# Kernel tuning notes

Measured on AMD Instinct MI355X. Metric: run time of the kernel, lower is better.

Reference implementation:

```python
import jax, jax.numpy as jnp
import numpy as np

B, D_IN, D_OUT, E, K, H = 8192, 1024, 1024, 8, 2, 2048


def setup_inputs() -> dict:
    key = jax.random.key(0)
    ks = jax.random.split(key, 7)
    s_in = 1.0 / np.sqrt(D_IN)
    s_h = 1.0 / np.sqrt(H)
    return {
        "x": jax.random.normal(ks[0], (B, D_IN), dtype=jnp.float32),
        "Wg": jax.random.uniform(ks[1], (D_IN, E), minval=-s_in, maxval=s_in, dtype=jnp.float32),
        "bg": jax.random.uniform(ks[2], (E,), minval=-s_in, maxval=s_in, dtype=jnp.float32),
        "W1": jax.random.uniform(ks[3], (E, D_IN, H), minval=-s_in, maxval=s_in, dtype=jnp.float32),
        "b1": jax.random.uniform(ks[4], (E, H), minval=-s_in, maxval=s_in, dtype=jnp.float32),
        "W2": jax.random.uniform(ks[5], (E, H, D_OUT), minval=-s_h, maxval=s_h, dtype=jnp.float32),
        "b2": jax.random.uniform(ks[6], (E, D_OUT), minval=-s_h, maxval=s_h, dtype=jnp.float32),
    }


def reference(x, Wg, bg, W1, b1, W2, b2):
    # gating: linear then top-k -> binary mask (scores are NOT used as weights)
    gate_scores = x @ Wg + bg                      # [B, E]
    _, topk_idx = jax.lax.top_k(gate_scores, K)    # [B, K]
    mask = jax.nn.one_hot(topk_idx, E, dtype=x.dtype).sum(axis=-2)  # [B, E]

    # dense compute of ALL experts (faithful to original module)
    h = jax.nn.relu(jnp.einsum('bi,eih->beh', x, W1) + b1[None])    # [B, E, H]
    expert_out = jnp.einsum('beh,eho->beo', h, W2) + b2[None]       # [B, E, D_OUT]

    # mask to top-k experts and sum over experts
    return jnp.einsum('beo,be->bo', expert_out, mask)               # [B, D_OUT]
```

## Files before the change

### kernel.cpp

```cpp
#include <hip/hip_runtime.h>


#define NTOK 8192
#define DIN  1024
#define DOUT 1024
#define NEXP 8
#define NHID 2048
#define NENT (NTOK * 2)
#define ABLK 64
#define MCHMAX 72

typedef __bf16 bf16_t;
typedef __bf16 bf16x8 __attribute__((ext_vector_type(8)));
typedef __bf16 bf16x4 __attribute__((ext_vector_type(4)));
typedef float  f32x4  __attribute__((ext_vector_type(4)));

#define AS3(p) ((__attribute__((address_space(3))) void*)(unsigned)(unsigned long long)(p))
#define AS1(p) ((__attribute__((address_space(1))) void*)(unsigned long long)(p))

static __device__ __forceinline__ int imin_(int a, int b) { return a < b ? a : b; }

static __device__ __forceinline__ int xcd_swizzle() {
    int cpx = gridDim.x >> 3;
    return (blockIdx.x & 7) * cpx + (blockIdx.x >> 3);
}

__global__ __launch_bounds__(256) void k_transpose_cvt(
    const float* __restrict__ W, bf16_t* __restrict__ WT, int K_, int N_)
{
    __shared__ float tile[64][65];
    const int tilesK = K_ >> 6, tilesN = N_ >> 6;
    int bid = blockIdx.x;
    int e = bid / (tilesK * tilesN);
    int r = bid % (tilesK * tilesN);
    int tk = (r / tilesN) << 6;
    int tn = (r % tilesN) << 6;
    const float* Wb  = W  + (size_t)e * K_ * N_;
    bf16_t*      WTb = WT + (size_t)e * K_ * N_;
    int lr = threadIdx.x >> 6;
    int lc = threadIdx.x & 63;
#pragma unroll
    for (int i = 0; i < 16; ++i) {
        int row = i * 4 + lr;
        tile[row][lc] = Wb[(size_t)(tk + row) * N_ + tn + lc];
    }
    __syncthreads();
#pragma unroll
    for (int i = 0; i < 16; ++i) {
        int row = i * 4 + lr;
        WTb[(size_t)(tn + row) * K_ + tk + lc] = (bf16_t)tile[lc][row];
    }
}

__global__ __launch_bounds__(256) void k_wgT(
    const float* __restrict__ Wg, float* __restrict__ WgT)
{
    int i = blockIdx.x * 256 + threadIdx.x;
    int d = i >> 3, e = i & 7;
    WgT[e * DIN + d] = Wg[i];
}

__global__ __launch_bounds__(256) void k_gating(
    const float* __restrict__ x, const float* __restrict__ WgT,
    const float* __restrict__ bg, bf16_t* __restrict__ xb,
    int* __restrict__ topk)
{
    int lane = threadIdx.x & 63;
    int tok  = blockIdx.x * 4 + (threadIdx.x >> 6);
    const float* xr  = x  + (size_t)tok * DIN;
    bf16_t*      xbr = xb + (size_t)tok * DIN;

    float4 xv[4];
#pragma unroll
    for (int i = 0; i < 4; ++i) {
        int idx = i * 256 + lane * 4;
        xv[i] = *reinterpret_cast<const float4*>(xr + idx);
        bf16x4 o;
        o[0] = (bf16_t)xv[i].x; o[1] = (bf16_t)xv[i].y;
        o[2] = (bf16_t)xv[i].z; o[3] = (bf16_t)xv[i].w;
        *reinterpret_cast<bf16x4*>(xbr + idx) = o;
    }

    float acc[NEXP];
#pragma unroll
    for (int e = 0; e < NEXP; ++e) {
        const float* we = WgT + (size_t)e * DIN;
        float a = 0.f;
#pragma unroll
        for (int i = 0; i < 4; ++i) {
            int idx = i * 256 + lane * 4;
            float4 w = *reinterpret_cast<const float4*>(we + idx);
            a += xv[i].x * w.x + xv[i].y * w.y + xv[i].z * w.z + xv[i].w * w.w;
        }
        acc[e] = a;
    }

#pragma unroll
    for (int e = 0; e < NEXP; ++e) {
#pragma unroll
        for (int off = 32; off >= 1; off >>= 1) acc[e] += __shfl_xor(acc[e], off);
    }
    if (lane == 0) {
        float s[NEXP];
#pragma unroll
        for (int e = 0; e < NEXP; ++e) s[e] = acc[e] + bg[e];
        int e0 = 0;
        for (int e = 1; e < NEXP; ++e) if (s[e] > s[e0]) e0 = e;
        int e1 = (e0 == 0) ? 1 : 0;
        for (int e = 0; e < NEXP; ++e) if (e != e0 && s[e] > s[e1]) e1 = e;
        topk[2 * tok]     = e0;
        topk[2 * tok + 1] = e1;
    }
}

__global__ __launch_bounds__(256) void k_hist(
    const int* __restrict__ topk, int* __restrict__ bh)
{
    __shared__ int h[NEXP];
    if (threadIdx.x < NEXP) h[threadIdx.x] = 0;
    __syncthreads();
    int i = blockIdx.x * 256 + threadIdx.x;
    atomicAdd(&h[topk[i]], 1);
    __syncthreads();
    if (threadIdx.x < NEXP) bh[blockIdx.x * NEXP + threadIdx.x] = h[threadIdx.x];
}

__global__ void k_scan2(const int* __restrict__ bh, int* __restrict__ counts,
                        int* __restrict__ offsets, int* __restrict__ blockbase,
                        int* __restrict__ chtab, int* __restrict__ nch)
{
    __shared__ int sc[NEXP], so_[NEXP + 1];
    int t = threadIdx.x;
    if (t < NEXP) {
        int s = 0;
        for (int b = 0; b < ABLK; ++b) s += bh[b * NEXP + t];
        sc[t] = s;
    }
    __syncthreads();
    if (t == 0) {
        int s = 0;
        for (int e = 0; e < NEXP; ++e) { so_[e] = s; s += sc[e]; }
        so_[NEXP] = s;
        for (int e = 0; e <= NEXP; ++e) offsets[e] = so_[e];
        for (int e = 0; e < NEXP; ++e) counts[e] = sc[e];
    }
    __syncthreads();
    if (t < NEXP) {
        int run = so_[t];
        for (int b = 0; b < ABLK; ++b) {
            blockbase[b * NEXP + t] = run;
            run += bh[b * NEXP + t];
        }
    }
    __syncthreads();
    if (t == 0) {
        int n = 0;
        for (int e = 0; e < NEXP; ++e) {
            int mch = (sc[e] + 255) >> 8;
            for (int m = 0; m < mch; ++m) chtab[n++] = (e << 16) | m;
        }
        nch[0] = n;
    }
}

__global__ __launch_bounds__(256) void k_assign(
    const int* __restrict__ topk, const int* __restrict__ blockbase,
    int* __restrict__ token_ids, int* __restrict__ slot_of)
{
    __shared__ int wcnt[4][NEXP];
    int tid = threadIdx.x, blk = blockIdx.x;
    int i = blk * 256 + tid;
    int e = topk[i];
    int lane = tid & 63, w = tid >> 6;
    unsigned long long ltmask = (1ull << lane) - 1ull;
    int rank_w = 0;
#pragma unroll
    for (int ee = 0; ee < NEXP; ++ee) {
        unsigned long long m = __ballot(e == ee);
        if (ee == e) rank_w = (int)__popcll(m & ltmask);
        if (lane == 0) wcnt[w][ee] = (int)__popcll(m);
    }
    __syncthreads();
    int pre = 0;
    for (int wv = 0; wv < w; ++wv) pre += wcnt[wv][e];
    int s = blockbase[blk * NEXP + e] + pre + rank_w;
    token_ids[s] = i >> 1;
    slot_of[i] = s;
}


#define GEMM_PHASES(NKV)                                                           \
    for (int kt = 0; kt < NKV; ++kt) {                                             \
        const short* Ac = &As[kt & 1][0][0];                                       \
        const short* Bc = &Bs[kt & 1][0][0];                                       \
        unsigned dstb = (unsigned)(((kt & 1) ^ 1) * 32768) + wb;                   \
        bf16x8 b_[4][2];                                                           \
        _Pragma("unroll")                                                          \
        for (int ph = 0; ph < 4; ++ph) {                                           \
            if (ph == 0) {                                                         \
                if (kt + 1 < NKV) {                                                \
                    int ko = (kt + 1) * 64;                                        \
                    __builtin_amdgcn_global_load_lds(AS1(aP0 + ko), AS3(AB + dstb),         16, 0, 0); \
                    __builtin_amdgcn_global_load_lds(AS1(aP1 + ko), AS3(AB + dstb + 8192),  16, 0, 0); \
                    __builtin_amdgcn_global_load_lds(AS1(aP2 + ko), AS3(AB + dstb + 16384), 16, 0, 0); \
                    __builtin_amdgcn_global_load_lds(AS1(aP3 + ko), AS3(AB + dstb + 24576), 16, 0, 0); \
                    __builtin_amdgcn_global_load_lds(AS1(bP0 + ko), AS3(BB + dstb),         16, 0, 0); \
                    __builtin_amdgcn_global_load_lds(AS1(bP1 + ko), AS3(BB + dstb + 8192),  16, 0, 0); \
                    __builtin_amdgcn_global_load_lds(AS1(bP2 + ko), AS3(BB + dstb + 16384), 16, 0, 0); \
                    __builtin_amdgcn_global_load_lds(AS1(bP3 + ko), AS3(BB + dstb + 24576), 16, 0, 0); \
                }                                                                  \
                _Pragma("unroll")                                                  \
                for (int nf = 0; nf < 4; ++nf) {                                   \
                    b_[nf][0] = *reinterpret_cast<const bf16x8*>(Bc + nf * 1024 + boff0);        \
                    b_[nf][1] = *reinterpret_cast<const bf16x8*>(Bc + nf * 1024 + (boff0 ^ 32)); \
                }                                                                  \
            }                                                                      \
            bf16x8 a_[2][2];                                                       \
            _Pragma("unroll")                                                      \
            for (int j = 0; j < 2; ++j) {                                          \
                const short* ar = Ac + (ph * 2 + j) * 1024;                        \
                a_[j][0] = *reinterpret_cast<const bf16x8*>(ar + aoff0);           \
                a_[j][1] = *reinterpret_cast<const bf16x8*>(ar + (aoff0 ^ 32));    \
            }                                                                      \
            __builtin_amdgcn_s_barrier();                                          \
            __builtin_amdgcn_s_setprio(1);                                         \
            _Pragma("unroll")                                                      \
            for (int j = 0; j < 2; ++j) {                                          \
                _Pragma("unroll")                                                  \
                for (int nf = 0; nf < 4; ++nf) {                                   \
                    acc[ph * 2 + j][nf] = __builtin_amdgcn_mfma_f32_16x16x32_bf16( \
                        a_[j][0], b_[nf][0], acc[ph * 2 + j][nf], 0, 0, 0);        \
                    acc[ph * 2 + j][nf] = __builtin_amdgcn_mfma_f32_16x16x32_bf16( \
                        a_[j][1], b_[nf][1], acc[ph * 2 + j][nf], 0, 0, 0);        \
                }                                                                  \
            }                                                                      \
            __builtin_amdgcn_s_setprio(0);                                         \
            if (ph == 3) asm volatile("s_waitcnt vmcnt(0)" ::: "memory");          \
            __builtin_amdgcn_s_barrier();                                          \
        }                                                                          \
    }

__global__ __launch_bounds__(512) void k_gemm1(
    const bf16_t* __restrict__ xb, const bf16_t* __restrict__ w1t,
    const float* __restrict__ b1, bf16_t* __restrict__ hb,
    const int* __restrict__ token_ids, const int* __restrict__ counts,
    const int* __restrict__ offsets, const int* __restrict__ chtab,
    const int* __restrict__ nch)
{
    int bid   = xcd_swizzle();
    int chunk = bid >> 3;
    int nc    = bid & 7;
    if (chunk >= nch[0]) return;
    int em = chtab[chunk];
    int e  = em >> 16;
    int mc = em & 0xffff;
    int count = counts[e];
    int base  = offsets[e];

    __shared__ short As[2][256][64];
    __shared__ short Bs[2][256][64];

    int t    = threadIdx.x;
    int w    = t >> 6;
    int lane = t & 63;
    int wrM  = (w >> 2) * 128;
    int wcN  = (w & 3) * 64;
    int lm   = lane & 15;
    int kq   = lane >> 4;
    int ru   = lane & 7;

    int aoff0 = (wrM + lm) * 64 + ((kq ^ ru) * 8);
    int boff0 = (wcN + lm) * 64 + ((kq ^ ru) * 8);

    int rbase = t >> 3;
    int c0s   = ((t & 7) ^ ((t >> 3) & 7)) * 8;
    unsigned wb = (unsigned)(w * 1024);

    const bf16_t* wgt = w1t + (size_t)e * NHID * DIN;
    int r0 = imin_(mc * 256 +   0 + rbase, count - 1);
    int r1 = imin_(mc * 256 +  64 + rbase, count - 1);
    int r2 = imin_(mc * 256 + 128 + rbase, count - 1);
    int r3 = imin_(mc * 256 + 192 + rbase, count - 1);
    const bf16_t* aP0 = xb + (size_t)token_ids[base + r0] * DIN + c0s;
    const bf16_t* aP1 = xb + (size_t)token_ids[base + r1] * DIN + c0s;
    const bf16_t* aP2 = xb + (size_t)token_ids[base + r2] * DIN + c0s;
    const bf16_t* aP3 = xb + (size_t)token_ids[base + r3] * DIN + c0s;
    const bf16_t* bP0 = wgt + (size_t)(nc * 256 +   0 + rbase) * DIN + c0s;
    const bf16_t* bP1 = wgt + (size_t)(nc * 256 +  64 + rbase) * DIN + c0s;
    const bf16_t* bP2 = wgt + (size_t)(nc * 256 + 128 + rbase) * DIN + c0s;
    const bf16_t* bP3 = wgt + (size_t)(nc * 256 + 192 + rbase) * DIN + c0s;

    char* AB = (char*)&As[0][0][0];
    char* BB = (char*)&Bs[0][0][0];

    f32x4 acc[8][4];
#pragma unroll
    for (int m = 0; m < 8; ++m)
#pragma unroll
        for (int n = 0; n < 4; ++n) acc[m][n] = (f32x4){0.f, 0.f, 0.f, 0.f};

    __builtin_amdgcn_global_load_lds(AS1(aP0), AS3(AB + wb),         16, 0, 0);
    __builtin_amdgcn_global_load_lds(AS1(aP1), AS3(AB + wb + 8192),  16, 0, 0);
    __builtin_amdgcn_global_load_lds(AS1(aP2), AS3(AB + wb + 16384), 16, 0, 0);
    __builtin_amdgcn_global_load_lds(AS1(aP3), AS3(AB + wb + 24576), 16, 0, 0);
    __builtin_amdgcn_global_load_lds(AS1(bP0), AS3(BB + wb),         16, 0, 0);
    __builtin_amdgcn_global_load_lds(AS1(bP1), AS3(BB + wb + 8192),  16, 0, 0);
    __builtin_amdgcn_global_load_lds(AS1(bP2), AS3(BB + wb + 16384), 16, 0, 0);
    __builtin_amdgcn_global_load_lds(AS1(bP3), AS3(BB + wb + 24576), 16, 0, 0);
    asm volatile("s_waitcnt vmcnt(0)" ::: "memory");
    __builtin_amdgcn_s_barrier();

    constexpr int NK = DIN / 64;
    GEMM_PHASES(NK)

    int rq = kq * 4;
#pragma unroll
    for (int nf = 0; nf < 4; ++nf) {
        int col  = nc * 256 + wcN + nf * 16 + lm;
        float bias = b1[e * NHID + col];
#pragma unroll
        for (int mf = 0; mf < 8; ++mf) {
            int gr0 = mc * 256 + wrM + mf * 16 + rq;
#pragma unroll
            for (int q = 0; q < 4; ++q) {
                int gr = gr0 + q;
                if (gr < count) {
                    float v = acc[mf][nf][q] + bias;
                    v = v > 0.f ? v : 0.f;
                    hb[(size_t)(base + gr) * NHID + col] = (bf16_t)v;
                }
            }
        }
    }
}

__global__ __launch_bounds__(512) void k_gemm2(
    const bf16_t* __restrict__ hb, const bf16_t* __restrict__ w2t,
    bf16_t* __restrict__ so,
    const int* __restrict__ counts, const int* __restrict__ offsets,
    const int* __restrict__ chtab, const int* __restrict__ nch)
{
    int bid   = xcd_swizzle();
    int chunk = bid >> 2;
    int nc    = bid & 3;
    if (chunk >= nch[0]) return;
    int em = chtab[chunk];
    int e  = em >> 16;
    int mc = em & 0xffff;
    int count = counts[e];
    int base  = offsets[e];

    __shared__ short As[2][256][64];
    __shared__ short Bs[2][256][64];

    int t    = threadIdx.x;
    int w    = t >> 6;
    int lane = t & 63;
    int wrM  = (w >> 2) * 128;
    int wcN  = (w & 3) * 64;
    int lm   = lane & 15;
    int kq   = lane >> 4;
    int ru   = lane & 7;

    int aoff0 = (wrM + lm) * 64 + ((kq ^ ru) * 8);
    int boff0 = (wcN + lm) * 64 + ((kq ^ ru) * 8);

    int rbase = t >> 3;
    int c0s   = ((t & 7) ^ ((t >> 3) & 7)) * 8;
    unsigned wb = (unsigned)(w * 1024);

    const bf16_t* wgt = w2t + (size_t)e * DOUT * NHID;
    int r0 = imin_(mc * 256 +   0 + rbase, count - 1);
    int r1 = imin_(mc * 256 +  64 + rbase, count - 1);
    int r2 = imin_(mc * 256 + 128 + rbase, count - 1);
    int r3 = imin_(mc * 256 + 192 + rbase, count - 1);
    const bf16_t* aP0 = hb + (size_t)(base + r0) * NHID + c0s;
    const bf16_t* aP1 = hb + (size_t)(base + r1) * NHID + c0s;
    const bf16_t* aP2 = hb + (size_t)(base + r2) * NHID + c0s;
    const bf16_t* aP3 = hb + (size_t)(base + r3) * NHID + c0s;
    const bf16_t* bP0 = wgt + (size_t)(nc * 256 +   0 + rbase) * NHID + c0s;
    const bf16_t* bP1 = wgt + (size_t)(nc * 256 +  64 + rbase) * NHID + c0s;
    const bf16_t* bP2 = wgt + (size_t)(nc * 256 + 128 + rbase) * NHID + c0s;
    const bf16_t* bP3 = wgt + (size_t)(nc * 256 + 192 + rbase) * NHID + c0s;

    char* AB = (char*)&As[0][0][0];
    char* BB = (char*)&Bs[0][0][0];

    f32x4 acc[8][4];
#pragma unroll
    for (int m = 0; m < 8; ++m)
#pragma unroll
        for (int n = 0; n < 4; ++n) acc[m][n] = (f32x4){0.f, 0.f, 0.f, 0.f};

    __builtin_amdgcn_global_load_lds(AS1(aP0), AS3(AB + wb),         16, 0, 0);
    __builtin_amdgcn_global_load_lds(AS1(aP1), AS3(AB + wb + 8192),  16, 0, 0);
    __builtin_amdgcn_global_load_lds(AS1(aP2), AS3(AB + wb + 16384), 16, 0, 0);
    __builtin_amdgcn_global_load_lds(AS1(aP3), AS3(AB + wb + 24576), 16, 0, 0);
    __builtin_amdgcn_global_load_lds(AS1(bP0), AS3(BB + wb),         16, 0, 0);
    __builtin_amdgcn_global_load_lds(AS1(bP1), AS3(BB + wb + 8192),  16, 0, 0);
    __builtin_amdgcn_global_load_lds(AS1(bP2), AS3(BB + wb + 16384), 16, 0, 0);
    __builtin_amdgcn_global_load_lds(AS1(bP3), AS3(BB + wb + 24576), 16, 0, 0);
    asm volatile("s_waitcnt vmcnt(0)" ::: "memory");
    __builtin_amdgcn_s_barrier();

    constexpr int NK = NHID / 64;
    GEMM_PHASES(NK)

    int rq = kq * 4;
#pragma unroll
    for (int nf = 0; nf < 4; ++nf) {
        int col = nc * 256 + wcN + nf * 16 + lm;
#pragma unroll
        for (int mf = 0; mf < 8; ++mf) {
            int gr0 = mc * 256 + wrM + mf * 16 + rq;
#pragma unroll
            for (int q = 0; q < 4; ++q) {
                int gr = gr0 + q;
                if (gr < count)
                    so[(size_t)(base + gr) * DOUT + col] = (bf16_t)acc[mf][nf][q];
            }
        }
    }
}

__global__ __launch_bounds__(256) void k_combine(
    const bf16_t* __restrict__ so, const float* __restrict__ b2,
    const int* __restrict__ topk, const int* __restrict__ slot_of,
    float* __restrict__ out)
{
    int tid = threadIdx.x;
    int tok = blockIdx.x * 2 + (tid >> 7);
    int c0  = (tid & 127) * 8;
    int s0 = slot_of[2 * tok],  s1 = slot_of[2 * tok + 1];
    int e0 = topk[2 * tok],     e1 = topk[2 * tok + 1];
    bf16x8 a = *reinterpret_cast<const bf16x8*>(so + (size_t)s0 * DOUT + c0);
    bf16x8 b = *reinterpret_cast<const bf16x8*>(so + (size_t)s1 * DOUT + c0);
    const float* bb0 = b2 + (size_t)e0 * DOUT + c0;
    const float* bb1 = b2 + (size_t)e1 * DOUT + c0;
    float* op = out + (size_t)tok * DOUT + c0;
    float4 o0, o1;
    o0.x = (float)a[0] + (float)b[0] + bb0[0] + bb1[0];
    o0.y = (float)a[1] + (float)b[1] + bb0[1] + bb1[1];
    o0.z = (float)a[2] + (float)b[2] + bb0[2] + bb1[2];
    o0.w = (float)a[3] + (float)b[3] + bb0[3] + bb1[3];
    o1.x = (float)a[4] + (float)b[4] + bb0[4] + bb1[4];
    o1.y = (float)a[5] + (float)b[5] + bb0[5] + bb1[5];
    o1.z = (float)a[6] + (float)b[6] + bb0[6] + bb1[6];
    o1.w = (float)a[7] + (float)b[7] + bb0[7] + bb1[7];
    *reinterpret_cast<float4*>(op)     = o0;
    *reinterpret_cast<float4*>(op + 4) = o1;
}

extern "C" void kernel_launch(void* const* d_in, const int* in_sizes, int n_in,
                              void* d_out, int out_size, void* d_ws, size_t ws_size,
                              hipStream_t stream)
{
    const float* x  = (const float*)d_in[0];
    const float* Wg = (const float*)d_in[1];
    const float* bg = (const float*)d_in[2];
    const float* W1 = (const float*)d_in[3];
    const float* b1 = (const float*)d_in[4];
    const float* W2 = (const float*)d_in[5];
    const float* b2 = (const float*)d_in[6];
    float* out = (float*)d_out;

    char* ws = (char*)d_ws;
    bf16_t* xb        = (bf16_t*)(ws);
    bf16_t* w1t       = (bf16_t*)(ws + 16777216);
    bf16_t* w2t       = (bf16_t*)(ws + 50331648);
    bf16_t* hb        = (bf16_t*)(ws + 83886080);
    int*    topk      = (int*)(ws + 150994944);
    int*    counts    = (int*)(ws + 151060480);
    int*    offsets   = (int*)(ws + 151060544);
    int*    token_ids = (int*)(ws + 151060608);
    int*    bh        = (int*)(ws + 151126144);
    int*    blockbase = (int*)(ws + 151128192);
    int*    slot_of   = (int*)(ws + 151130240);

    int* chtab = bh;
    int* nch   = bh + MCHMAX;

    bf16_t* so = (bf16_t*)ws;
    float* wgT = (float*)hb;

    k_wgT<<<(DIN * NEXP) / 256, 256, 0, stream>>>(Wg, wgT);

    k_transpose_cvt<<<NEXP * (DIN / 64) * (NHID / 64), 256, 0, stream>>>(W1, w1t, DIN, NHID);
    k_transpose_cvt<<<NEXP * (NHID / 64) * (DOUT / 64), 256, 0, stream>>>(W2, w2t, NHID, DOUT);

    k_gating<<<NTOK / 4, 256, 0, stream>>>(x, wgT, bg, xb, topk);
    k_hist<<<ABLK, 256, 0, stream>>>(topk, bh);
    k_scan2<<<1, 64, 0, stream>>>(bh, counts, offsets, blockbase, chtab, nch);
    k_assign<<<ABLK, 256, 0, stream>>>(topk, blockbase, token_ids, slot_of);

    k_gemm1<<<MCHMAX * 8, 512, 0, stream>>>(
        xb, w1t, b1, hb, token_ids, counts, offsets, chtab, nch);
    k_gemm2<<<MCHMAX * 4, 512, 0, stream>>>(
        hb, w2t, so, counts, offsets, chtab, nch);
    k_combine<<<NTOK / 2, 256, 0, stream>>>(so, b2, topk, slot_of, out);
}
```

Baseline: 337.2 us.

## Replace double-buffered phased GEMM pipeline with single-buffer load-sync-compute loop

Both expert GEMM kernels drop the double-buffered LDS tiles and the four-phase interleaved prefetch/MFMA schedule with setprio. They now use one LDS buffer per operand, loading each K tile, synchronizing, computing, and synchronizing again. This halves LDS usage, which may allow more resident blocks, but it serializes global-to-LDS loads with the MFMA work instead of overlapping them. The __syncthreads after the async global_load_lds may also not wait on vmcnt, which risks reading incomplete tiles.

```diff
diff --git a/kernel.cpp b/kernel.cpp
--- a/kernel.cpp
+++ b/kernel.cpp
@@ -189,57 +189,6 @@
 }
 
 
-#define GEMM_PHASES(NKV)                                                           \
-    for (int kt = 0; kt < NKV; ++kt) {                                             \
-        const short* Ac = &As[kt & 1][0][0];                                       \
-        const short* Bc = &Bs[kt & 1][0][0];                                       \
-        unsigned dstb = (unsigned)(((kt & 1) ^ 1) * 32768) + wb;                   \
-        bf16x8 b_[4][2];                                                           \
-        _Pragma("unroll")                                                          \
-        for (int ph = 0; ph < 4; ++ph) {                                           \
-            if (ph == 0) {                                                         \
-                if (kt + 1 < NKV) {                                                \
-                    int ko = (kt + 1) * 64;                                        \
-                    __builtin_amdgcn_global_load_lds(AS1(aP0 + ko), AS3(AB + dstb),         16, 0, 0); \
-                    __builtin_amdgcn_global_load_lds(AS1(aP1 + ko), AS3(AB + dstb + 8192),  16, 0, 0); \
-                    __builtin_amdgcn_global_load_lds(AS1(aP2 + ko), AS3(AB + dstb + 16384), 16, 0, 0); \
-                    __builtin_amdgcn_global_load_lds(AS1(aP3 + ko), AS3(AB + dstb + 24576), 16, 0, 0); \
-                    __builtin_amdgcn_global_load_lds(AS1(bP0 + ko), AS3(BB + dstb),         16, 0, 0); \
-                    __builtin_amdgcn_global_load_lds(AS1(bP1 + ko), AS3(BB + dstb + 8192),  16, 0, 0); \
-                    __builtin_amdgcn_global_load_lds(AS1(bP2 + ko), AS3(BB + dstb + 16384), 16, 0, 0); \
-                    __builtin_amdgcn_global_load_lds(AS1(bP3 + ko), AS3(BB + dstb + 24576), 16, 0, 0); \
-                }                                                                  \
-                _Pragma("unroll")                                                  \
-                for (int nf = 0; nf < 4; ++nf) {                                   \
-                    b_[nf][0] = *reinterpret_cast<const bf16x8*>(Bc + nf * 1024 + boff0);        \
-                    b_[nf][1] = *reinterpret_cast<const bf16x8*>(Bc + nf * 1024 + (boff0 ^ 32)); \
-                }                                                                  \
-            }                                                                      \
-            bf16x8 a_[2][2];                                                       \
-            _Pragma("unroll")                                                      \
-            for (int j = 0; j < 2; ++j) {                                          \
-                const short* ar = Ac + (ph * 2 + j) * 1024;                        \
-                a_[j][0] = *reinterpret_cast<const bf16x8*>(ar + aoff0);           \
-                a_[j][1] = *reinterpret_cast<const bf16x8*>(ar + (aoff0 ^ 32));    \
-            }                                                                      \
-            __builtin_amdgcn_s_barrier();                                          \
-            __builtin_amdgcn_s_setprio(1);                                         \
-            _Pragma("unroll")                                                      \
-            for (int j = 0; j < 2; ++j) {                                          \
-                _Pragma("unroll")                                                  \
-                for (int nf = 0; nf < 4; ++nf) {                                   \
-                    acc[ph * 2 + j][nf] = __builtin_amdgcn_mfma_f32_16x16x32_bf16( \
-                        a_[j][0], b_[nf][0], acc[ph * 2 + j][nf], 0, 0, 0);        \
-                    acc[ph * 2 + j][nf] = __builtin_amdgcn_mfma_f32_16x16x32_bf16( \
-                        a_[j][1], b_[nf][1], acc[ph * 2 + j][nf], 0, 0, 0);        \
-                }                                                                  \
-            }                                                                      \
-            __builtin_amdgcn_s_setprio(0);                                         \
-            if (ph == 3) asm volatile("s_waitcnt vmcnt(0)" ::: "memory");          \
-            __builtin_amdgcn_s_barrier();                                          \
-        }                                                                          \
-    }
-
 __global__ __launch_bounds__(512) void k_gemm1(
     const bf16_t* __restrict__ xb, const bf16_t* __restrict__ w1t,
     const float* __restrict__ b1, bf16_t* __restrict__ hb,
@@ -257,8 +206,8 @@
     int count = counts[e];
     int base  = offsets[e];
 
-    __shared__ short As[2][256][64];
-    __shared__ short Bs[2][256][64];
+    __shared__ short As[256][64];
+    __shared__ short Bs[256][64];
 
     int t    = threadIdx.x;
     int w    = t >> 6;
@@ -290,8 +239,10 @@
     const bf16_t* bP2 = wgt + (size_t)(nc * 256 + 128 + rbase) * DIN + c0s;
     const bf16_t* bP3 = wgt + (size_t)(nc * 256 + 192 + rbase) * DIN + c0s;
 
-    char* AB = (char*)&As[0][0][0];
-    char* BB = (char*)&Bs[0][0][0];
+    char* AB = (char*)&As[0][0];
+    char* BB = (char*)&Bs[0][0];
+    const short* Ac = &As[0][0];
+    const short* Bc = &Bs[0][0];
 
     f32x4 acc[8][4];
 #pragma unroll
@@ -299,19 +250,38 @@
 #pragma unroll
         for (int n = 0; n < 4; ++n) acc[m][n] = (f32x4){0.f, 0.f, 0.f, 0.f};
 
-    __builtin_amdgcn_global_load_lds(AS1(aP0), AS3(AB + wb),         16, 0, 0);
-    __builtin_amdgcn_global_load_lds(AS1(aP1), AS3(AB + wb + 8192),  16, 0, 0);
-    __builtin_amdgcn_global_load_lds(AS1(aP2), AS3(AB + wb + 16384), 16, 0, 0);
-    __builtin_amdgcn_global_load_lds(AS1(aP3), AS3(AB + wb + 24576), 16, 0, 0);
-    __builtin_amdgcn_global_load_lds(AS1(bP0), AS3(BB + wb),         16, 0, 0);
-    __builtin_amdgcn_global_load_lds(AS1(bP1), AS3(BB + wb + 8192),  16, 0, 0);
-    __builtin_amdgcn_global_load_lds(AS1(bP2), AS3(BB + wb + 16384), 16, 0, 0);
-    __builtin_amdgcn_global_load_lds(AS1(bP3), AS3(BB + wb + 24576), 16, 0, 0);
-    asm volatile("s_waitcnt vmcnt(0)" ::: "memory");
-    __builtin_amdgcn_s_barrier();
-
     constexpr int NK = DIN / 64;
-    GEMM_PHASES(NK)
+    for (int kt = 0; kt < NK; ++kt) {
+        int ko = kt * 64;
+        __builtin_amdgcn_global_load_lds(AS1(aP0 + ko), AS3(AB + wb),         16, 0, 0);
+        __builtin_amdgcn_global_load_lds(AS1(aP1 + ko), AS3(AB + wb + 8192),  16, 0, 0);
+        __builtin_amdgcn_global_load_lds(AS1(aP2 + ko), AS3(AB + wb + 16384), 16, 0, 0);
+        __builtin_amdgcn_global_load_lds(AS1(aP3 + ko), AS3(AB + wb + 24576), 16, 0, 0);
+        __builtin_amdgcn_global_load_lds(AS1(bP0 + ko), AS3(BB + wb),         16, 0, 0);
+        __builtin_amdgcn_global_load_lds(AS1(bP1 + ko), AS3(BB + wb + 8192),  16, 0, 0);
+        __builtin_amdgcn_global_load_lds(AS1(bP2 + ko), AS3(BB + wb + 16384), 16, 0, 0);
+        __builtin_amdgcn_global_load_lds(AS1(bP3 + ko), AS3(BB + wb + 24576), 16, 0, 0);
+        __syncthreads();
+
+        bf16x8 b_[4][2];
+#pragma unroll
+        for (int nf = 0; nf < 4; ++nf) {
+            b_[nf][0] = *reinterpret_cast<const bf16x8*>(Bc + nf * 1024 + boff0);
+            b_[nf][1] = *reinterpret_cast<const bf16x8*>(Bc + nf * 1024 + (boff0 ^ 32));
+        }
+#pragma unroll
+        for (int mf = 0; mf < 8; ++mf) {
+            const short* ar = Ac + mf * 1024;
+            bf16x8 a0 = *reinterpret_cast<const bf16x8*>(ar + aoff0);
+            bf16x8 a1 = *reinterpret_cast<const bf16x8*>(ar + (aoff0 ^ 32));
+#pragma unroll
+            for (int nf = 0; nf < 4; ++nf) {
+                acc[mf][nf] = __builtin_amdgcn_mfma_f32_16x16x32_bf16(a0, b_[nf][0], acc[mf][nf], 0, 0, 0);
+                acc[mf][nf] = __builtin_amdgcn_mfma_f32_16x16x32_bf16(a1, b_[nf][1], acc[mf][nf], 0, 0, 0);
+            }
+        }
+        __syncthreads();
+    }
 
     int rq = kq * 4;
 #pragma unroll
@@ -350,8 +320,8 @@
     int count = counts[e];
     int base  = offsets[e];
 
-    __shared__ short As[2][256][64];
-    __shared__ short Bs[2][256][64];
+    __shared__ short As[256][64];
+    __shared__ short Bs[256][64];
 
     int t    = threadIdx.x;
     int w    = t >> 6;
@@ -383,8 +353,10 @@
     const bf16_t* bP2 = wgt + (size_t)(nc * 256 + 128 + rbase) * NHID + c0s;
     const bf16_t* bP3 = wgt + (size_t)(nc * 256 + 192 + rbase) * NHID + c0s;
 
-    char* AB = (char*)&As[0][0][0];
-    char* BB = (char*)&Bs[0][0][0];
+    char* AB = (char*)&As[0][0];
+    char* BB = (char*)&Bs[0][0];
+    const short* Ac = &As[0][0];
+    const short* Bc = &Bs[0][0];
 
     f32x4 acc[8][4];
 #pragma unroll
@@ -392,19 +364,38 @@
 #pragma unroll
         for (int n = 0; n < 4; ++n) acc[m][n] = (f32x4){0.f, 0.f, 0.f, 0.f};
 
-    __builtin_amdgcn_global_load_lds(AS1(aP0), AS3(AB + wb),         16, 0, 0);
-    __builtin_amdgcn_global_load_lds(AS1(aP1), AS3(AB + wb + 8192),  16, 0, 0);
-    __builtin_amdgcn_global_load_lds(AS1(aP2), AS3(AB + wb + 16384), 16, 0, 0);
-    __builtin_amdgcn_global_load_lds(AS1(aP3), AS3(AB + wb + 24576), 16, 0, 0);
-    __builtin_amdgcn_global_load_lds(AS1(bP0), AS3(BB + wb),         16, 0, 0);
-    __builtin_amdgcn_global_load_lds(AS1(bP1), AS3(BB + wb + 8192),  16, 0, 0);
-    __builtin_amdgcn_global_load_lds(AS1(bP2), AS3(BB + wb + 16384), 16, 0, 0);
-    __builtin_amdgcn_global_load_lds(AS1(bP3), AS3(BB + wb + 24576), 16, 0, 0);
-    asm volatile("s_waitcnt vmcnt(0)" ::: "memory");
-    __builtin_amdgcn_s_barrier();
-
     constexpr int NK = NHID / 64;
-    GEMM_PHASES(NK)
+    for (int kt = 0; kt < NK; ++kt) {
+        int ko = kt * 64;
+        __builtin_amdgcn_global_load_lds(AS1(aP0 + ko), AS3(AB + wb),         16, 0, 0);
+        __builtin_amdgcn_global_load_lds(AS1(aP1 + ko), AS3(AB + wb + 8192),  16, 0, 0);
+        __builtin_amdgcn_global_load_lds(AS1(aP2 + ko), AS3(AB + wb + 16384), 16, 0, 0);
+        __builtin_amdgcn_global_load_lds(AS1(aP3 + ko), AS3(AB + wb + 24576), 16, 0, 0);
+        __builtin_amdgcn_global_load_lds(AS1(bP0 + ko), AS3(BB + wb),         16, 0, 0);
+        __builtin_amdgcn_global_load_lds(AS1(bP1 + ko), AS3(BB + wb + 8192),  16, 0, 0);
+        __builtin_amdgcn_global_load_lds(AS1(bP2 + ko), AS3(BB + wb + 16384), 16, 0, 0);
+        __builtin_amdgcn_global_load_lds(AS1(bP3 + ko), AS3(BB + wb + 24576), 16, 0, 0);
+        __syncthreads();
+
+        bf16x8 b_[4][2];
+#pragma unroll
+        for (int nf = 0; nf < 4; ++nf) {
+            b_[nf][0] = *reinterpret_cast<const bf16x8*>(Bc + nf * 1024 + boff0);
+            b_[nf][1] = *reinterpret_cast<const bf16x8*>(Bc + nf * 1024 + (boff0 ^ 32));
+        }
+#pragma unroll
+        for (int mf = 0; mf < 8; ++mf) {
+            const short* ar = Ac + mf * 1024;
+            bf16x8 a0 = *reinterpret_cast<const bf16x8*>(ar + aoff0);
+            bf16x8 a1 = *reinterpret_cast<const bf16x8*>(ar + (aoff0 ^ 32));
+#pragma unroll
+            for (int nf = 0; nf < 4; ++nf) {
+                acc[mf][nf] = __builtin_amdgcn_mfma_f32_16x16x32_bf16(a0, b_[nf][0], acc[mf][nf], 0, 0, 0);
+                acc[mf][nf] = __builtin_amdgcn_mfma_f32_16x16x32_bf16(a1, b_[nf][1], acc[mf][nf], 0, 0, 0);
+            }
+        }
+        __syncthreads();
+    }
 
     int rq = kq * 4;
 #pragma unroll
```

Measured after the change: 363.9 us. +7.9%, slower.
